# Kernel tuning notes

Hardware: AMD Instinct MI355X
Metric: run time of the kernel (lower is better)

Reference implementation:

```python
import jax, jax.numpy as jnp
import numpy as np

BN_EPS = 1e-5

def conv2d(x, w, pad):
    return jax.lax.conv_general_dilated(x, w, (1, 1), [(pad, pad), (pad, pad)],
                                        dimension_numbers=('NCHW', 'OIHW', 'NCHW'))

def bn(x, g, b, m, v):
    # eval-mode batchnorm with running stats
    c = (None, slice(None), None, None)
    return g[c] * (x - m[c]) * jax.lax.rsqrt(v[c] + BN_EPS) + b[c]

def criss_cross_attention(x, wq, wk, wv, gamma):
    # x: (B, C, H, W); q/k have reduced dim d = C//8
    B, C, H, W = x.shape
    q = jnp.einsum('bchw,dc->bdhw', x, wq)
    k = jnp.einsum('bchw,dc->bdhw', x, wk)
    v = jnp.einsum('bchw,dc->bdhw', x, wv)
    # column (vertical) affinities: for each (h,w), keys at (k,w) -> (B,H,W,H)
    eH = jnp.einsum('bdhw,bdkw->bhwk', q, k)
    # -inf on the h==k diagonal (avoid counting the center pixel twice)
    eH = eH + jnp.where(jnp.eye(H, dtype=bool), -jnp.inf, 0.0)[None, :, None, :]
    # row (horizontal) affinities: keys at (h,k) -> (B,H,W,W)
    eW = jnp.einsum('bdhw,bdhk->bhwk', q, k)
    att = jax.nn.softmax(jnp.concatenate([eH, eW], axis=3), axis=3)  # (B,H,W,H+W)
    aH, aW = att[..., :H], att[..., H:]
    oH = jnp.einsum('bhwk,bdkw->bdhw', aH, v)
    oW = jnp.einsum('bhwk,bdhk->bdhw', aW, v)
    return gamma * (oH + oW) + x

def upsample_bilinear_align_corners(x, out_h, out_w):
    # torch nn.Upsample(mode='bilinear', align_corners=True)
    def interp(x, size, axis):
        n = x.shape[axis]
        pos = jnp.arange(size, dtype=x.dtype) * ((n - 1) / (size - 1))
        lo = jnp.floor(pos).astype(jnp.int32)
        hi = jnp.minimum(lo + 1, n - 1)
        w = pos - lo.astype(x.dtype)
        shp = [1] * x.ndim; shp[axis] = size
        w = w.reshape(shp)
        return jnp.take(x, lo, axis=axis) * (1 - w) + jnp.take(x, hi, axis=axis) * w
    x = interp(x, out_h, 2)
    return interp(x, out_w, 3)

def setup_inputs() -> dict:
    key = jax.random.key(0)
    ks = jax.random.split(key, 16)
    B, C, H, W = 2, 2048, 96, 96
    ic = C // 32          # inter_c = 64
    dq = ic // 8          # 8
    nc = 19
    s = 0.05
    return {
        'x': jax.random.normal(ks[0], (B, C, H, W), jnp.float32),
        'w_in': jax.random.normal(ks[1], (ic, C, 3, 3), jnp.float32) * s,
        'bn_in_g': jnp.ones((ic,), jnp.float32),
        'bn_in_b': jnp.zeros((ic,), jnp.float32),
        'bn_in_m': jax.random.normal(ks[2], (ic,), jnp.float32) * 0.1,
        'bn_in_v': jax.random.uniform(ks[3], (ic,), jnp.float32, 0.5, 1.5),
        'wq': jax.random.normal(ks[4], (dq, ic), jnp.float32) * s,
        'wk': jax.random.normal(ks[5], (dq, ic), jnp.float32) * s,
        'wv': jax.random.normal(ks[6], (ic, ic), jnp.float32) * s,
        'cca_gamma': jax.random.uniform(ks[7], (1,), jnp.float32, 0.2, 0.8),
        'w_out': jax.random.normal(ks[8], (ic, ic, 3, 3), jnp.float32) * s,
        'bn_out_g': jnp.ones((ic,), jnp.float32),
        'bn_out_b': jnp.zeros((ic,), jnp.float32),
        'bn_out_m': jax.random.normal(ks[9], (ic,), jnp.float32) * 0.1,
        'bn_out_v': jax.random.uniform(ks[10], (ic,), jnp.float32, 0.5, 1.5),
        'w_cls1': jax.random.normal(ks[11], (ic, C + ic, 3, 3), jnp.float32) * s,
        'bn_cls_g': jnp.ones((ic,), jnp.float32),
        'bn_cls_b': jnp.zeros((ic,), jnp.float32),
        'bn_cls_m': jax.random.normal(ks[12], (ic,), jnp.float32) * 0.1,
        'bn_cls_v': jax.random.uniform(ks[13], (ic,), jnp.float32, 0.5, 1.5),
        'w_cls2': jax.random.normal(ks[14], (nc, ic, 1, 1), jnp.float32) * s,
    }

def reference(x, w_in, bn_in_g, bn_in_b, bn_in_m, bn_in_v,
              wq, wk, wv, cca_gamma,
              w_out, bn_out_g, bn_out_b, bn_out_m, bn_out_v,
              w_cls1, bn_cls_g, bn_cls_b, bn_cls_m, bn_cls_v, w_cls2):
    RECURRENCE = 2
    out = jax.nn.relu(bn(conv2d(x, w_in, 1), bn_in_g, bn_in_b, bn_in_m, bn_in_v))
    for _ in range(RECURRENCE):
        out = criss_cross_attention(out, wq, wk, wv, cca_gamma)
    out = jax.nn.relu(bn(conv2d(out, w_out, 1), bn_out_g, bn_out_b, bn_out_m, bn_out_v))
    out = jnp.concatenate([x, out], axis=1)
    # cls_seg: conv -> BN (no relu) -> upsample x8 (bilinear, align_corners) -> 1x1 conv
    out = bn(conv2d(out, w_cls1, 1), bn_cls_g, bn_cls_b, bn_cls_m, bn_cls_v)
    H, W = out.shape[2], out.shape[3]
    out = upsample_bilinear_align_corners(out, H * 8, W * 8)
    out = conv2d(out, w_cls2, 0)
    return out
```

## Files before the change

kernel.cpp:

```cpp
#include <hip/hip_runtime.h>
#include <stdint.h>

#define HW 9216

typedef float f32x4 __attribute__((ext_vector_type(4)));
typedef short s16x8 __attribute__((ext_vector_type(8)));

#define PIN() asm volatile("" ::: "memory")
#define WAITV12() asm volatile("s_waitcnt vmcnt(12)" ::: "memory")

__device__ __forceinline__ unsigned short f2bf(float f){
  union { float fv; uint32_t u; } x; x.fv = f;
  uint32_t u = x.u;
  u += 0x7fffu + ((u >> 16) & 1u);
  return (unsigned short)(u >> 16);
}
__device__ __forceinline__ float bf2f(unsigned short s){
  union { uint32_t u; float fv; } x; x.u = ((uint32_t)s) << 16;
  return x.fv;
}

__device__ __forceinline__ void gload16(const void* g, void* l){
  __builtin_amdgcn_global_load_lds(
    (const __attribute__((address_space(1))) unsigned int*)g,
    (__attribute__((address_space(3))) unsigned int*)l, 16, 0, 0);
}

__global__ __launch_bounds__(256) void transp_kernel(const float* __restrict__ x,
    unsigned short* __restrict__ xT){
  __shared__ unsigned short tl[256 * 66];
  int blk = blockIdx.x;
  int b = blk / 1152; int r = blk - b * 1152;
  int cchunk = r / 144, pxt = r - cchunk * 144;
  int c0 = cchunk * 256, px0 = pxt * 64;
  int tid = threadIdx.x;
  for (int e = tid; e < 4096; e += 256){
    int cc = e >> 4, pq = e & 15;
    float4 v4 = *(const float4*)(x + ((size_t)(b * 2048 + c0 + cc)) * HW + px0 + pq * 4);
    const float* vp = (const float*)&v4;
    #pragma unroll
    for (int j = 0; j < 4; j++) tl[cc * 66 + pq * 4 + j] = f2bf(vp[j]);
  }
  __syncthreads();
  for (int j = tid; j < 2048; j += 256){
    int px = j >> 5, oct = j & 31;
    s16x8 pk;
    #pragma unroll
    for (int t = 0; t < 8; t++) pk[t] = (short)tl[(oct * 8 + t) * 66 + px];
    *(s16x8*)(xT + ((size_t)(b * 9216 + px0 + px)) * 2048 + c0 + oct * 8) = pk;
  }
}

__global__ void packw_kernel(const float* __restrict__ w, unsigned short* __restrict__ Wp, int Cin){
  int total = 64 * Cin * 9;
  for (int i = blockIdx.x * blockDim.x + threadIdx.x; i < total; i += gridDim.x * blockDim.x){
    int c = i & 31; int r = i >> 5; int o = r & 63; int r2 = r >> 6;
    int tap = r2 % 9; int ck = r2 / 9;
    Wp[i] = f2bf(w[((size_t)o * Cin + ck * 32 + c) * 9 + tap]);
  }
}

template<int T>
__device__ __forceinline__ void tapbody(const char* hb, s16x8 (&bs)[4], f32x4 (&acc)[4][4],
    const unsigned short* wbase, int gmax, int g0, int wv, int ln, int kg){
  constexpr int dy = T / 3, dx = T - dy * 3;
  #pragma unroll
  for (int mf = 0; mf < 4; mf++){
    int p = (wv * 4 + mf + dy) * 18 + (ln + dx);
    int aoff = p * 64 + ((kg ^ (p & 3)) << 4);
    s16x8 a = *(const s16x8*)(hb + aoff);
    #pragma unroll
    for (int nf = 0; nf < 4; nf++)
      acc[mf][nf] = __builtin_amdgcn_mfma_f32_16x16x32_bf16(a, bs[nf], acc[mf][nf], 0, 0, 0);
  }
  constexpr int dck = (T + 3) / 9, dt = (T + 3) % 9;
  if (g0 + T + 3 < gmax){
    const unsigned short* wb2 = wbase + dck * 18432 + dt * 2048;
    #pragma unroll
    for (int nf = 0; nf < 4; nf++) bs[nf] = *(const s16x8*)(wb2 + nf * 512);
  }
}

__global__ __launch_bounds__(256, 2) void conv_nhwc_kernel(
    const unsigned short* __restrict__ A0, int c0stride,
    const unsigned short* __restrict__ A1, int nck0,
    const unsigned short* __restrict__ Wp,
    unsigned short* __restrict__ sl, int nchunks,
    const unsigned short* __restrict__ zp){
  int mt = blockIdx.x;
  int b = mt / 36; int r = mt - b * 36;
  int h0 = (r / 6) * 16, w0 = (r % 6) * 16;
  int KS = gridDim.y, ks = blockIdx.y;
  int c0 = (nchunks * ks) / KS, c1 = (nchunks * (ks + 1)) / KS;
  int tid = threadIdx.x, lane = tid & 63, wv = tid >> 6;
  int ln = lane & 15, kg = lane >> 4;
  __shared__ char halo[2][24576];

  int pixb0[6], pixb1[6]; bool val[6];
  #pragma unroll
  for (int rr = 0; rr < 6; rr++){
    int i = tid + rr * 256;
    int p = i >> 2, q_lds = i & 3;
    int logq = q_lds ^ (p & 3);
    int hh = p / 18, ww = p - hh * 18;
    int h = h0 - 1 + hh, w = w0 - 1 + ww;
    bool v = (i < 1296) && ((unsigned)h < 96u) && ((unsigned)w < 96u);
    val[rr] = v;
    int pix = (b * 96 + h) * 96 + w;
    pixb0[rr] = v ? (pix * c0stride * 2 + logq * 16) : 0;
    pixb1[rr] = v ? (pix * 128 + logq * 16) : 0;
  }
  const char* a0B = (const char*)A0;
  const char* a1B = (const char*)A1;
  const char* zpB = (const char*)zp;

  auto stage = [&](char* ldsB, int ck){
    bool inA0 = (ck < nck0);
    int chb0 = ck * 64, chb1 = (ck - nck0) * 64;
    #pragma unroll
    for (int rr = 0; rr < 6; rr++){
      const char* src = zpB;
      if (val[rr]) src = inA0 ? (a0B + pixb0[rr] + chb0) : (a1B + pixb1[rr] + chb1);
      gload16(src, ldsB + (tid + rr * 256) * 16);
    }
  };

  f32x4 acc[4][4];
  #pragma unroll
  for (int i = 0; i < 4; i++)
    #pragma unroll
    for (int j = 0; j < 4; j++) acc[i][j] = (f32x4)(0.f);

  s16x8 bs0[4], bs1[4], bs2[4];
  int gmax = (c1 - c0) * 9;

  stage(&halo[0][0], c0);
  PIN();
  {
    const unsigned short* w0b = Wp + (size_t)c0 * 18432 + ln * 32 + kg * 8;
    #pragma unroll
    for (int nf = 0; nf < 4; nf++){
      bs0[nf] = *(const s16x8*)(w0b + 0 * 2048 + nf * 512);
      bs1[nf] = *(const s16x8*)(w0b + 1 * 2048 + nf * 512);
      bs2[nf] = *(const s16x8*)(w0b + 2 * 2048 + nf * 512);
    }
  }
  WAITV12();
  __builtin_amdgcn_s_barrier();

  for (int ck = c0; ck < c1; ck++){
    int cur = (ck - c0) & 1;
    if (ck + 1 < c1){ stage(&halo[cur ^ 1][0], ck + 1); PIN(); }
    const unsigned short* wbase = Wp + (size_t)ck * 18432 + ln * 32 + kg * 8;
    const char* hb = &halo[cur][0];
    int g0 = (ck - c0) * 9;
    tapbody<0>(hb, bs0, acc, wbase, gmax, g0, wv, ln, kg);
    tapbody<1>(hb, bs1, acc, wbase, gmax, g0, wv, ln, kg);
    tapbody<2>(hb, bs2, acc, wbase, gmax, g0, wv, ln, kg);
    tapbody<3>(hb, bs0, acc, wbase, gmax, g0, wv, ln, kg);
    tapbody<4>(hb, bs1, acc, wbase, gmax, g0, wv, ln, kg);
    tapbody<5>(hb, bs2, acc, wbase, gmax, g0, wv, ln, kg);
    tapbody<6>(hb, bs0, acc, wbase, gmax, g0, wv, ln, kg);
    tapbody<7>(hb, bs1, acc, wbase, gmax, g0, wv, ln, kg);
    tapbody<8>(hb, bs2, acc, wbase, gmax, g0, wv, ln, kg);
    if (ck + 1 < c1){
      WAITV12();
      __builtin_amdgcn_s_barrier();
    }
  }

  unsigned short* base = sl + ((size_t)(ks * 72 + mt)) * 16384;
  #pragma unroll
  for (int mf = 0; mf < 4; mf++)
    #pragma unroll
    for (int nf = 0; nf < 4; nf++){
      int o = nf * 16 + ln;
      #pragma unroll
      for (int rr = 0; rr < 4; rr++){
        int m = wv * 64 + mf * 16 + kg * 4 + rr;
        base[m * 64 + o] = f2bf(acc[mf][nf][rr]);
      }
    }
}

__global__ __launch_bounds__(256) void bn_reduce_kernel(const unsigned short* __restrict__ sl,
    int KS, const float* __restrict__ g, const float* __restrict__ bb,
    const float* __restrict__ mm, const float* __restrict__ vv, int relu,
    unsigned short* __restrict__ out){
  int idx = blockIdx.x * 256 + threadIdx.x;
  int mt = idx >> 14, e = idx & 16383;
  int m = e >> 6, o = e & 63;
  float s = 0.f;
  for (int ks = 0; ks < KS; ks++) s += bf2f(sl[((size_t)(ks * 72 + mt)) * 16384 + e]);
  float sc = g[o] * rsqrtf(vv[o] + 1e-5f);
  float valf = (s - mm[o]) * sc + bb[o];
  if (relu) valf = fmaxf(valf, 0.f);
  int b = mt / 36; int r = mt - b * 36;
  int h = (r / 6) * 16 + (m >> 4), w = (r % 6) * 16 + (m & 15);
  out[(((size_t)b * 96 + h) * 96 + w) * 64 + o] = f2bf(valf);
}

__global__ __launch_bounds__(256) void bn_reduce_cls_kernel(const unsigned short* __restrict__ sl,
    int KS, const float* __restrict__ g, const float* __restrict__ bb,
    const float* __restrict__ mm, const float* __restrict__ vv,
    const float* __restrict__ w2, float* __restrict__ t19){
  __shared__ float yl[4][64];
  __shared__ float w2L[19 * 64];
  int tid = threadIdx.x;
  for (int i = tid; i < 1216; i += 256) w2L[i] = w2[i];
  int idx = blockIdx.x * 256 + tid;
  int mt = idx >> 14, e = idx & 16383;
  int o = e & 63;
  float s = 0.f;
  for (int ks = 0; ks < KS; ks++) s += bf2f(sl[((size_t)(ks * 72 + mt)) * 16384 + e]);
  float sc = g[o] * rsqrtf(vv[o] + 1e-5f);
  float valf = (s - mm[o]) * sc + bb[o];
  yl[tid >> 6][o] = valf;
  __syncthreads();
  if (tid < 76){
    int mq = tid / 19, j = tid - mq * 19;
    float a = 0.f;
    #pragma unroll 8
    for (int c = 0; c < 64; c++) a += w2L[j * 64 + c] * yl[mq][c];
    int m = ((blockIdx.x & 63) << 2) + mq;
    int b = mt / 36; int r = mt - b * 36;
    int h = (r / 6) * 16 + (m >> 4), w = (r % 6) * 16 + (m & 15);
    t19[((size_t)(b * 19 + j)) * HW + h * 96 + w] = a;
  }
}

__global__ __launch_bounds__(256) void cca_proj_kernel(const unsigned short* __restrict__ xin,
    const float* __restrict__ wq, const float* __restrict__ wk, const float* __restrict__ wv,
    float* __restrict__ q, float* __restrict__ k, float* __restrict__ v){
  __shared__ float wqL[512], wkL[512], wvL[4096];
  int tid = threadIdx.x;
  for (int i = tid; i < 512; i += 256){ wqL[i] = wq[i]; wkL[i] = wk[i]; }
  for (int i = tid; i < 4096; i += 256) wvL[i] = wv[i];
  __syncthreads();
  int gid = blockIdx.x * 256 + tid;
  int gp = gid >> 1, half = gid & 1;
  unsigned short xv16[64];
  #pragma unroll
  for (int t = 0; t < 8; t++)
    *(s16x8*)(&xv16[t * 8]) = *(const s16x8*)(xin + (size_t)gp * 64 + t * 8);
  float qa[4], ka[4], va[32];
  #pragma unroll
  for (int d = 0; d < 4; d++){ qa[d] = 0.f; ka[d] = 0.f; }
  #pragma unroll
  for (int d = 0; d < 32; d++) va[d] = 0.f;
  int qo = half * 4, vo = half * 32;
  #pragma unroll 4
  for (int c = 0; c < 64; c++){
    float xv = bf2f(xv16[c]);
    #pragma unroll
    for (int d = 0; d < 4; d++){ qa[d] += wqL[(qo + d) * 64 + c] * xv; ka[d] += wkL[(qo + d) * 64 + c] * xv; }
    #pragma unroll
    for (int d = 0; d < 32; d++) va[d] += wvL[(vo + d) * 64 + c] * xv;
  }
  #pragma unroll
  for (int d = 0; d < 4; d++){ q[(size_t)gp * 8 + qo + d] = qa[d]; k[(size_t)gp * 8 + qo + d] = ka[d]; }
  #pragma unroll
  for (int d = 0; d < 32; d++) v[(size_t)gp * 64 + vo + d] = va[d];
}

__global__ __launch_bounds__(256, 2) void cca_colE_kernel(const float* __restrict__ qT,
    const float* __restrict__ kT, float* __restrict__ ebuf){
  int blk = blockIdx.x;
  int b = blk / 192; int r = blk - b * 192; int w = r >> 1, z = r & 1;
  __shared__ float qcL[96 * 12], kcL[48 * 12];
  int tid = threadIdx.x;
  for (int i = tid; i < 768; i += 256){
    int hp = i >> 3, d = i & 7;
    qcL[hp * 12 + d] = qT[((size_t)(b * HW) + hp * 96 + w) * 8 + d];
  }
  for (int i = tid; i < 384; i += 256){
    int j = i >> 3, d = i & 7;
    kcL[j * 12 + d] = kT[((size_t)(b * HW) + (z * 48 + j) * 96 + w) * 8 + d];
  }
  __syncthreads();
  int h0 = (tid & 15) * 6, kl0 = (tid >> 4) * 3;
  f32x4 q0[6], q1[6], k0[3], k1[3];
  #pragma unroll
  for (int i = 0; i < 6; i++){
    q0[i] = *(const f32x4*)&qcL[(h0 + i) * 12];
    q1[i] = *(const f32x4*)&qcL[(h0 + i) * 12 + 4];
  }
  #pragma unroll
  for (int j = 0; j < 3; j++){
    k0[j] = *(const f32x4*)&kcL[(kl0 + j) * 12];
    k1[j] = *(const f32x4*)&kcL[(kl0 + j) * 12 + 4];
  }
  #pragma unroll
  for (int i = 0; i < 6; i++){
    size_t rbase = (((size_t)b * 96 + (h0 + i)) * 96 + w) * 96;
    #pragma unroll
    for (int j = 0; j < 3; j++){
      float e = 0.f;
      #pragma unroll
      for (int d = 0; d < 4; d++) e += q0[i][d] * k0[j][d] + q1[i][d] * k1[j][d];
      int kpg = z * 48 + kl0 + j;
      ebuf[rbase + kpg] = (kpg == h0 + i) ? -1e30f : e;
    }
  }
}

__global__ __launch_bounds__(256, 2) void cca_rowSM_kernel(const float* __restrict__ qT,
    const float* __restrict__ kT, const float* __restrict__ vT,
    const unsigned short* __restrict__ xin, const float* __restrict__ gamma,
    float* __restrict__ ebuf, unsigned short* __restrict__ xout){
  int blk = blockIdx.x;
  int b = blk / 192; int r = blk - b * 192; int h = r >> 1, z = r & 1;
  __shared__ float qrL[48 * 12], krL[96 * 12];
  __shared__ float ewT[96 * 50];
  __shared__ unsigned short vL2[96 * 68];
  __shared__ unsigned short aW[96 * 50];
  int tid = threadIdx.x;
  int lane = tid & 63, wvid = tid >> 6;
  size_t rowb = (size_t)(b * HW) + h * 96;
  const float* ebase = ebuf + rowb * 96;

  float pre0[12], pre1[12];
  #pragma unroll
  for (int t = 0; t < 12; t++){
    int w = z * 48 + wvid + t * 4;
    pre0[t] = ebase[(size_t)w * 96 + lane];
    pre1[t] = (lane < 32) ? ebase[(size_t)w * 96 + 64 + lane] : 0.f;
  }

  for (int i = tid; i < 384; i += 256){
    int wl = i >> 3, d = i & 7;
    qrL[wl * 12 + d] = qT[(rowb + z * 48 + wl) * 8 + d];
  }
  for (int i = tid; i < 768; i += 256){
    int wp = i >> 3, d = i & 7;
    krL[wp * 12 + d] = kT[(rowb + wp) * 8 + d];
  }
  for (int i = tid; i < 6144; i += 256){
    int wp = i >> 6, d = i & 63;
    vL2[wp * 68 + d] = f2bf(vT[(rowb + wp) * 64 + d]);
  }
  __syncthreads();
  {
    int wl0 = (tid & 15) * 3, kp0 = (tid >> 4) * 6;
    f32x4 q0[3], q1[3], k0[6], k1[6];
    #pragma unroll
    for (int i = 0; i < 3; i++){
      q0[i] = *(const f32x4*)&qrL[(wl0 + i) * 12];
      q1[i] = *(const f32x4*)&qrL[(wl0 + i) * 12 + 4];
    }
    #pragma unroll
    for (int j = 0; j < 6; j++){
      k0[j] = *(const f32x4*)&krL[(kp0 + j) * 12];
      k1[j] = *(const f32x4*)&krL[(kp0 + j) * 12 + 4];
    }
    #pragma unroll
    for (int j = 0; j < 6; j++)
      #pragma unroll
      for (int i = 0; i < 3; i++){
        float e = 0.f;
        #pragma unroll
        for (int d = 0; d < 4; d++) e += q0[i][d] * k0[j][d] + q1[i][d] * k1[j][d];
        ewT[(kp0 + j) * 50 + (wl0 + i)] = e;
      }
  }
  __syncthreads();
  #pragma unroll
  for (int t = 0; t < 12; t++){
    int wl = wvid + t * 4;
    int w = z * 48 + wl;
    float x0 = pre0[t];
    float x1 = (lane < 32) ? pre1[t] : ewT[(lane - 32) * 50 + wl];
    float x2 = ewT[(lane + 32) * 50 + wl];
    float mx = fmaxf(x0, fmaxf(x1, x2));
    #pragma unroll
    for (int s = 32; s; s >>= 1) mx = fmaxf(mx, __shfl_xor(mx, s));
    float e0 = __expf(x0 - mx), e1 = __expf(x1 - mx), e2 = __expf(x2 - mx);
    float sm = e0 + e1 + e2;
    #pragma unroll
    for (int s = 32; s; s >>= 1) sm += __shfl_xor(sm, s);
    float inv = 1.f / sm;
    float* ebw = (float*)(ebase + (size_t)w * 96);
    ebw[lane] = e0 * inv;
    if (lane < 32) ebw[64 + lane] = e1 * inv;
    else           aW[(lane - 32) * 50 + wl] = f2bf(e1 * inv);
    aW[(lane + 32) * 50 + wl] = f2bf(e2 * inv);
  }
  __syncthreads();
  float gm = gamma[0];
  int d0 = (tid & 15) * 4, wl0 = (tid >> 4) * 3;
  f32x4 acc2[3];
  #pragma unroll
  for (int c = 0; c < 3; c++) acc2[c] = (f32x4)(0.f);
  for (int kp = 0; kp < 96; kp++){
    ushort4 vv4 = *(const ushort4*)&vL2[kp * 68 + d0];
    f32x4 vf; vf[0] = bf2f(vv4.x); vf[1] = bf2f(vv4.y); vf[2] = bf2f(vv4.z); vf[3] = bf2f(vv4.w);
    acc2[0] += vf * bf2f(aW[kp * 50 + wl0]);
    acc2[1] += vf * bf2f(aW[kp * 50 + wl0 + 1]);
    acc2[2] += vf * bf2f(aW[kp * 50 + wl0 + 2]);
  }
  #pragma unroll
  for (int c = 0; c < 3; c++){
    size_t pix = rowb + z * 48 + wl0 + c;
    ushort4 xr = *(const ushort4*)&xin[pix * 64 + d0];
    ushort4 ov;
    ov.x = f2bf(bf2f(xr.x) + gm * acc2[c][0]);
    ov.y = f2bf(bf2f(xr.y) + gm * acc2[c][1]);
    ov.z = f2bf(bf2f(xr.z) + gm * acc2[c][2]);
    ov.w = f2bf(bf2f(xr.w) + gm * acc2[c][3]);
    *(ushort4*)&xout[pix * 64 + d0] = ov;
  }
}

__global__ __launch_bounds__(256, 2) void cca_colO_kernel(const float* __restrict__ vT,
    const float* __restrict__ gamma, const float* __restrict__ ebuf,
    const unsigned short* __restrict__ xpart, unsigned short* __restrict__ xout){
  int blk = blockIdx.x;
  int b = blk / 192; int r = blk - b * 192; int w = r >> 1, z = r & 1;
  __shared__ unsigned short vL2[96 * 68];
  __shared__ unsigned short aTb[96 * 50];
  int tid = threadIdx.x;
  for (int i = tid; i < 6144; i += 256){
    int kp = i >> 6, d = i & 63;
    vL2[kp * 68 + d] = f2bf(vT[((size_t)(b * HW) + kp * 96 + w) * 64 + d]);
  }
  for (int i = tid; i < 4608; i += 256){
    int hl = i / 96, kp = i - hl * 96;
    aTb[kp * 50 + hl] = f2bf(ebuf[(((size_t)b * 96 + z * 48 + hl) * 96 + w) * 96 + kp]);
  }
  __syncthreads();
  float gm = gamma[0];
  int d0 = (tid & 15) * 4, hl0 = (tid >> 4) * 3;
  f32x4 acc2[3];
  #pragma unroll
  for (int c = 0; c < 3; c++) acc2[c] = (f32x4)(0.f);
  for (int kp = 0; kp < 96; kp++){
    ushort4 vv4 = *(const ushort4*)&vL2[kp * 68 + d0];
    f32x4 vf; vf[0] = bf2f(vv4.x); vf[1] = bf2f(vv4.y); vf[2] = bf2f(vv4.z); vf[3] = bf2f(vv4.w);
    acc2[0] += vf * bf2f(aTb[kp * 50 + hl0]);
    acc2[1] += vf * bf2f(aTb[kp * 50 + hl0 + 1]);
    acc2[2] += vf * bf2f(aTb[kp * 50 + hl0 + 2]);
  }
  #pragma unroll
  for (int c = 0; c < 3; c++){
    size_t pix = (size_t)(b * HW) + (z * 48 + hl0 + c) * 96 + w;
    ushort4 xr = *(const ushort4*)&xpart[pix * 64 + d0];
    ushort4 ov;
    ov.x = f2bf(bf2f(xr.x) + gm * acc2[c][0]);
    ov.y = f2bf(bf2f(xr.y) + gm * acc2[c][1]);
    ov.z = f2bf(bf2f(xr.z) + gm * acc2[c][2]);
    ov.w = f2bf(bf2f(xr.w) + gm * acc2[c][3]);
    *(ushort4*)&xout[pix * 64 + d0] = ov;
  }
}

__global__ void upsample_kernel(const float* __restrict__ t19, float* __restrict__ out){
  int gid = blockIdx.x * 256 + threadIdx.x;
  int xq = gid % 192; int t = gid / 192;
  int yy = t % 768; t /= 768;
  int o = t % 19; int b = t / 19;
  const float R = 95.0f / 767.0f;
  float ry = yy * R;
  int iy = (int)ry;
  float fy = ry - (float)iy;
  int iy1 = min(iy + 1, 95);
  const float* base = t19 + ((size_t)b * 19 + o) * HW;
  float4 res;
  float* rp = (float*)&res;
  #pragma unroll
  for (int j = 0; j < 4; j++){
    int xx = xq * 4 + j;
    float rx = xx * R;
    int ix = (int)rx; float fx = rx - (float)ix; int ix1 = min(ix + 1, 95);
    float v00 = base[iy * 96 + ix],  v01 = base[iy * 96 + ix1];
    float v10 = base[iy1 * 96 + ix], v11 = base[iy1 * 96 + ix1];
    rp[j] = (1.f - fy) * ((1.f - fx) * v00 + fx * v01) + fy * ((1.f - fx) * v10 + fx * v11);
  }
  *(float4*)(out + (((size_t)b * 19 + o) * 768 + yy) * 768 + xq * 4) = res;
}

extern "C" void kernel_launch(void* const* d_in, const int* in_sizes, int n_in,
                              void* d_out, int out_size, void* d_ws, size_t ws_size,
                              hipStream_t stream){
  const float* x       = (const float*)d_in[0];
  const float* w_in    = (const float*)d_in[1];
  const float* bn_in_g = (const float*)d_in[2];
  const float* bn_in_b = (const float*)d_in[3];
  const float* bn_in_m = (const float*)d_in[4];
  const float* bn_in_v = (const float*)d_in[5];
  const float* wq      = (const float*)d_in[6];
  const float* wk      = (const float*)d_in[7];
  const float* wv      = (const float*)d_in[8];
  const float* gamma   = (const float*)d_in[9];
  const float* w_out   = (const float*)d_in[10];
  const float* bn_o_g  = (const float*)d_in[11];
  const float* bn_o_b  = (const float*)d_in[12];
  const float* bn_o_m  = (const float*)d_in[13];
  const float* bn_o_v  = (const float*)d_in[14];
  const float* w_cls1  = (const float*)d_in[15];
  const float* bn_c_g  = (const float*)d_in[16];
  const float* bn_c_b  = (const float*)d_in[17];
  const float* bn_c_m  = (const float*)d_in[18];
  const float* bn_c_v  = (const float*)d_in[19];
  const float* w_cls2  = (const float*)d_in[20];
  float* out = (float*)d_out;

  char* ws = (char*)d_ws;
  size_t off = 0;
  auto alloc = [&](size_t bytes) -> void* {
    void* p = ws + off; off += (bytes + 255) & ~(size_t)255; return p;
  };
  const int KS = 12;
  const size_t NHWCb = (size_t)2 * HW * 64 * 2;
  unsigned short* xT   = (unsigned short*)alloc((size_t)2 * HW * 2048 * 2);
  unsigned short* sl   = (unsigned short*)alloc((size_t)KS * 72 * 16384 * 2);
  float* ebuf = (float*)sl;
  unsigned short* xattA = (unsigned short*)alloc(NHWCb);
  unsigned short* xattB = (unsigned short*)alloc(NHWCb);
  unsigned short* Ptmp  = (unsigned short*)alloc(NHWCb);
  unsigned short* attT  = (unsigned short*)alloc(NHWCb);
  unsigned short* midT  = (unsigned short*)alloc(NHWCb);
  float* qb    = (float*)alloc((size_t)2 * HW * 8 * 4);
  float* kb    = (float*)alloc((size_t)2 * HW * 8 * 4);
  float* vb    = (float*)alloc((size_t)2 * HW * 64 * 4);
  float* t19   = (float*)alloc((size_t)2 * 19 * HW * 4);
  unsigned short* WpIn  = (unsigned short*)alloc((size_t)64 * 2048 * 9 * 2);
  unsigned short* WpOut = (unsigned short*)alloc((size_t)64 * 64 * 9 * 2);
  unsigned short* WpCls = (unsigned short*)alloc((size_t)64 * 2112 * 9 * 2);
  unsigned short* zp    = (unsigned short*)alloc(256);
  (void)ws_size; (void)in_sizes; (void)n_in; (void)out_size;

  hipMemsetAsync(zp, 0, 256, stream);
  transp_kernel<<<2304, 256, 0, stream>>>(x, xT);
  packw_kernel<<<1024, 256, 0, stream>>>(w_in,   WpIn,  2048);
  packw_kernel<<<64,   256, 0, stream>>>(w_out,  WpOut, 64);
  packw_kernel<<<1024, 256, 0, stream>>>(w_cls1, WpCls, 2112);

  conv_nhwc_kernel<<<dim3(72, KS), 256, 0, stream>>>(xT, 2048, nullptr, 64, WpIn, sl, 64, zp);
  bn_reduce_kernel<<<4608, 256, 0, stream>>>(sl, KS, bn_in_g, bn_in_b, bn_in_m, bn_in_v, 1, xattA);

  cca_proj_kernel<<<144, 256, 0, stream>>>(xattA, wq, wk, wv, qb, kb, vb);
  cca_colE_kernel<<<384, 256, 0, stream>>>(qb, kb, ebuf);
  cca_rowSM_kernel<<<384, 256, 0, stream>>>(qb, kb, vb, xattA, gamma, ebuf, Ptmp);
  cca_colO_kernel<<<384, 256, 0, stream>>>(vb, gamma, ebuf, Ptmp, xattB);
  cca_proj_kernel<<<144, 256, 0, stream>>>(xattB, wq, wk, wv, qb, kb, vb);
  cca_colE_kernel<<<384, 256, 0, stream>>>(qb, kb, ebuf);
  cca_rowSM_kernel<<<384, 256, 0, stream>>>(qb, kb, vb, xattB, gamma, ebuf, Ptmp);
  cca_colO_kernel<<<384, 256, 0, stream>>>(vb, gamma, ebuf, Ptmp, attT);

  conv_nhwc_kernel<<<dim3(72, 2), 256, 0, stream>>>(attT, 64, nullptr, 2, WpOut, sl, 2, zp);
  bn_reduce_kernel<<<4608, 256, 0, stream>>>(sl, 2, bn_o_g, bn_o_b, bn_o_m, bn_o_v, 1, midT);

  conv_nhwc_kernel<<<dim3(72, KS), 256, 0, stream>>>(xT, 2048, midT, 64, WpCls, sl, 66, zp);
  bn_reduce_cls_kernel<<<4608, 256, 0, stream>>>(sl, KS, bn_c_g, bn_c_b, bn_c_m, bn_c_v, w_cls2, t19);

  upsample_kernel<<<21888, 256, 0, stream>>>(t19, out);
}
```

Measured before the change: 453.3 us.

## Triple-buffer conv halo staging, raise split-K to 16, swizzle blocks across XCDs

The implicit-GEMM conv kernel now prefetches the input halo two channel chunks ahead using three LDS buffers instead of two, with the vmcnt waits adjusted to match. This aims to hide more global-load latency behind the MFMA work. The split-K factor for the two large convs goes from 12 to 16, and a 1D grid is remapped so that all blocks with the same K-split land on the same XCD, improving L2 reuse of weight chunks. The costs are extra LDS per block (72KB, which may limit occupancy to two blocks per CU) and more partial-sum traffic for the BN reduce.

```diff
diff --git a/kernel.cpp b/kernel.cpp
--- a/kernel.cpp
+++ b/kernel.cpp
@@ -8,6 +8,7 @@
 
 #define PIN() asm volatile("" ::: "memory")
 #define WAITV12() asm volatile("s_waitcnt vmcnt(12)" ::: "memory")
+#define WAITV18() asm volatile("s_waitcnt vmcnt(18)" ::: "memory")
 
 __device__ __forceinline__ unsigned short f2bf(float f){
   union { float fv; uint32_t u; } x; x.fv = f;
@@ -85,16 +86,22 @@
     const unsigned short* __restrict__ A0, int c0stride,
     const unsigned short* __restrict__ A1, int nck0,
     const unsigned short* __restrict__ Wp,
-    unsigned short* __restrict__ sl, int nchunks,
+    unsigned short* __restrict__ sl, int nchunks, int KS, int swz,
     const unsigned short* __restrict__ zp){
-  int mt = blockIdx.x;
+  int j = blockIdx.x;
+  int mt, ks;
+  if (swz){
+    int xcd = j & 7; int t = j >> 3;
+    ks = xcd + 8 * (t / 72); mt = t % 72;
+  } else {
+    mt = j % 72; ks = j / 72;
+  }
   int b = mt / 36; int r = mt - b * 36;
   int h0 = (r / 6) * 16, w0 = (r % 6) * 16;
-  int KS = gridDim.y, ks = blockIdx.y;
   int c0 = (nchunks * ks) / KS, c1 = (nchunks * (ks + 1)) / KS;
   int tid = threadIdx.x, lane = tid & 63, wv = tid >> 6;
   int ln = lane & 15, kg = lane >> 4;
-  __shared__ char halo[2][24576];
+  __shared__ char halo[3][24576];
 
   int pixb0[6], pixb1[6]; bool val[6];
   #pragma unroll
@@ -129,12 +136,14 @@
   #pragma unroll
   for (int i = 0; i < 4; i++)
     #pragma unroll
-    for (int j = 0; j < 4; j++) acc[i][j] = (f32x4)(0.f);
+    for (int j2 = 0; j2 < 4; j2++) acc[i][j2] = (f32x4)(0.f);
 
   s16x8 bs0[4], bs1[4], bs2[4];
   int gmax = (c1 - c0) * 9;
 
   stage(&halo[0][0], c0);
+  bool two = (c0 + 1 < c1);
+  if (two) stage(&halo[1][0], c0 + 1);
   PIN();
   {
     const unsigned short* w0b = Wp + (size_t)c0 * 18432 + ln * 32 + kg * 8;
@@ -145,14 +154,18 @@
       bs2[nf] = *(const s16x8*)(w0b + 2 * 2048 + nf * 512);
     }
   }
-  WAITV12();
+  if (two) WAITV18(); else WAITV12();
   __builtin_amdgcn_s_barrier();
 
+  int cur = 0;
   for (int ck = c0; ck < c1; ck++){
-    int cur = (ck - c0) & 1;
-    if (ck + 1 < c1){ stage(&halo[cur ^ 1][0], ck + 1); PIN(); }
+    if (ck + 2 < c1){
+      int nx2 = cur + 2; if (nx2 >= 3) nx2 -= 3;
+      stage(&halo[0][0] + nx2 * 24576, ck + 2);
+      PIN();
+    }
     const unsigned short* wbase = Wp + (size_t)ck * 18432 + ln * 32 + kg * 8;
-    const char* hb = &halo[cur][0];
+    const char* hb = &halo[0][0] + cur * 24576;
     int g0 = (ck - c0) * 9;
     tapbody<0>(hb, bs0, acc, wbase, gmax, g0, wv, ln, kg);
     tapbody<1>(hb, bs1, acc, wbase, gmax, g0, wv, ln, kg);
@@ -164,9 +177,10 @@
     tapbody<7>(hb, bs1, acc, wbase, gmax, g0, wv, ln, kg);
     tapbody<8>(hb, bs2, acc, wbase, gmax, g0, wv, ln, kg);
     if (ck + 1 < c1){
-      WAITV12();
+      if (ck + 2 < c1) WAITV18(); else WAITV12();
       __builtin_amdgcn_s_barrier();
     }
+    cur = cur + 1; if (cur >= 3) cur -= 3;
   }
 
   unsigned short* base = sl + ((size_t)(ks * 72 + mt)) * 16384;
@@ -509,7 +523,7 @@
   auto alloc = [&](size_t bytes) -> void* {
     void* p = ws + off; off += (bytes + 255) & ~(size_t)255; return p;
   };
-  const int KS = 12;
+  const int KS = 16;
   const size_t NHWCb = (size_t)2 * HW * 64 * 2;
   unsigned short* xT   = (unsigned short*)alloc((size_t)2 * HW * 2048 * 2);
   unsigned short* sl   = (unsigned short*)alloc((size_t)KS * 72 * 16384 * 2);
@@ -535,7 +549,7 @@
   packw_kernel<<<64,   256, 0, stream>>>(w_out,  WpOut, 64);
   packw_kernel<<<1024, 256, 0, stream>>>(w_cls1, WpCls, 2112);
 
-  conv_nhwc_kernel<<<dim3(72, KS), 256, 0, stream>>>(xT, 2048, nullptr, 64, WpIn, sl, 64, zp);
+  conv_nhwc_kernel<<<72 * KS, 256, 0, stream>>>(xT, 2048, nullptr, 64, WpIn, sl, 64, KS, 1, zp);
   bn_reduce_kernel<<<4608, 256, 0, stream>>>(sl, KS, bn_in_g, bn_in_b, bn_in_m, bn_in_v, 1, xattA);
 
   cca_proj_kernel<<<144, 256, 0, stream>>>(xattA, wq, wk, wv, qb, kb, vb);
@@ -547,10 +561,10 @@
   cca_rowSM_kernel<<<384, 256, 0, stream>>>(qb, kb, vb, xattB, gamma, ebuf, Ptmp);
   cca_colO_kernel<<<384, 256, 0, stream>>>(vb, gamma, ebuf, Ptmp, attT);
 
-  conv_nhwc_kernel<<<dim3(72, 2), 256, 0, stream>>>(attT, 64, nullptr, 2, WpOut, sl, 2, zp);
+  conv_nhwc_kernel<<<144, 256, 0, stream>>>(attT, 64, nullptr, 2, WpOut, sl, 2, 2, 0, zp);
   bn_reduce_kernel<<<4608, 256, 0, stream>>>(sl, 2, bn_o_g, bn_o_b, bn_o_m, bn_o_v, 1, midT);
 
-  conv_nhwc_kernel<<<dim3(72, KS), 256, 0, stream>>>(xT, 2048, midT, 64, WpCls, sl, 66, zp);
+  conv_nhwc_kernel<<<72 * KS, 256, 0, stream>>>(xT, 2048, midT, 64, WpCls, sl, 66, KS, 1, zp);
   bn_reduce_cls_kernel<<<4608, 256, 0, stream>>>(sl, KS, bn_c_g, bn_c_b, bn_c_m, bn_c_v, w_cls2, t19);
 
   upsample_kernel<<<21888, 256, 0, stream>>>(t19, out);
```

New measurement: 476.4 us. +5.1%, slower.
